# Optimization experiments

Hardware: AMD Instinct MI355X
Metric: run time of the kernel (lower is better)

Reference implementation:

```python
import jax, jax.numpy as jnp
import numpy as np

POSITIVE = 1e-6  # cfg.positive epsilon


def unnormal_gaussian(mask_shape, loc):
    """Unnormalized 2D gaussian per box. loc: [B,N,4] = (cx, cy, w, h) in [0,1].
    Returns [B, N, H, W]."""
    H, W = mask_shape
    cx, cy, w, h = loc[..., 0], loc[..., 1], loc[..., 2], loc[..., 3]
    xs = (jnp.arange(W, dtype=loc.dtype) + 0.5) / W  # [W]
    ys = (jnp.arange(H, dtype=loc.dtype) + 0.5) / H  # [H]
    sx = jnp.maximum(w, 1e-3)[..., None, None]  # [B,N,1,1]
    sy = jnp.maximum(h, 1e-3)[..., None, None]
    dx = xs[None, None, None, :] - cx[..., None, None]  # [B,N,1,W]
    dy = ys[None, None, :, None] - cy[..., None, None]  # [B,N,H,1]
    return jnp.exp(-(dx**2 / (2.0 * sx**2) + dy**2 / (2.0 * sy**2)))


def setup_inputs() -> dict:
    key = jax.random.key(0)
    k1, k2, k3, k4, k5 = jax.random.split(key, 5)
    B, N, K, Hp, Wp, C, H0, W0 = 8, 200, 32, 138, 138, 3, 550, 550
    return {
        "original": jax.random.normal(k1, (B, C, H0, W0), dtype=jnp.float32),
        "loc": jax.random.uniform(k2, (B, N, 4), dtype=jnp.float32),
        "mask": jax.random.normal(k3, (B, N, K), dtype=jnp.float32),
        "conf": jax.random.uniform(k4, (B, N), dtype=jnp.float32),
        "proto": jax.random.normal(k5, (B, Hp, Wp, K), dtype=jnp.float32),
    }


def reference(original, loc, mask, conf, proto):
    original = original.astype(jnp.float32)
    B, C, H0, W0 = original.shape
    Hp, Wp = proto.shape[1], proto.shape[2]
    K = proto.shape[3]

    # gaussian attention window per detection: [B,N,Hp,Wp]
    ug = unnormal_gaussian((Hp, Wp), loc)
    # lincomb of prototypes: [B,N,Hp,Wp]
    assembled = jnp.einsum("bhwk,bnk->bnhw", proto, mask)
    assembled = jax.nn.sigmoid(assembled)
    attention = assembled * ug
    # weight by per-detection confidence: [B,N,Hp,Wp]
    mask_conf = attention * conf[:, :, None, None]
    # normalized squared-confidence reduction over detections: [B,Hp,Wp]
    denom = jnp.sum(mask_conf, axis=1, keepdims=True) + POSITIVE
    final_conf = 1.0 - jnp.sum(mask_conf**2 / denom, axis=1)
    final_conf = jnp.where(jnp.isnan(final_conf), 0.0, final_conf)
    # bilinear resize (align_corners=False == half-pixel centers): [B,H0,W0]
    resized = jax.image.resize(final_conf[:, None], (B, 1, H0, W0), method="linear")[:, 0]
    total_conf = jnp.sum(resized, axis=0)  # [H0,W0]
    weighted_mean = jnp.einsum("bchw,bhw->chw", original, resized) / total_conf
    squared_diff = (original - weighted_mean[None]) ** 2
    weighted_diff = squared_diff * resized[:, None]  # einsum 'abcd,acd->abcd'
    weighted_var = weighted_diff / (total_conf + POSITIVE)
    return jnp.sum(weighted_var) / K * B
```

## Files before the change

### kernel.cpp

```cpp
#include <hip/hip_runtime.h>
#include <math.h>

#define BB   8
#define NDET 200
#define NDP  208
#define NCH  13
#define KK   32
#define HP   138
#define WP   138
#define NXT  9
#define NYP  69
#define NP   (HP*WP)
#define H0   550
#define W0   550
#define NPIX (H0*W0)
#define CC   3
#define POSEPS 1e-6f

typedef __attribute__((ext_vector_type(8))) short  short8;
typedef __attribute__((ext_vector_type(4))) float  floatx4;

#define OFF_AFRAG 0
#define OFF_GX    106496
#define OFF_GYC   1025024
#define OFF_FCONF 1943552

extern "C" __device__ float __builtin_amdgcn_rcpf(float);

__device__ inline unsigned short f32_to_bf16(float f) {
    union { float f; unsigned u; } v; v.f = f;
    unsigned r = v.u + 0x7FFFu + ((v.u >> 16) & 1u);
    return (unsigned short)(r >> 16);
}

__global__ __launch_bounds__(256) void prep_kernel(
    const float* __restrict__ loc,
    const float* __restrict__ conf,
    const float* __restrict__ mask,
    char* __restrict__ ws,
    float* __restrict__ out)
{
    const int idx = blockIdx.x * 256 + threadIdx.x;
    if (idx == 0) out[0] = 0.0f;
    const int W1 = BB * WP * NDP;
    const int W2 = BB * HP * NDP;
    if (idx < W1) {
        int b = idx / (WP * NDP); int r = idx - b * (WP * NDP);
        int x = r / NDP;          int n = r - x * NDP;
        float v = 0.0f;
        if (n < NDET) {
            const float* l = loc + (b * NDET + n) * 4;
            float cx = l[0];
            float w  = fmaxf(l[2], 1e-3f);
            float ia = 1.0f / (2.0f * w * w);
            float dx = (x + 0.5f) * (1.0f / WP) - cx;
            v = __expf(-dx * dx * ia);
        }
        ((float*)(ws + OFF_GX))[idx] = v;
    } else if (idx < W1 + W2) {
        int k = idx - W1;
        int b = k / (HP * NDP); int r = k - b * (HP * NDP);
        int y = r / NDP;        int n = r - y * NDP;
        float v = 0.0f;
        if (n < NDET) {
            const float* l = loc + (b * NDET + n) * 4;
            float cy = l[1];
            float h  = fmaxf(l[3], 1e-3f);
            float ib = 1.0f / (2.0f * h * h);
            float dy = (y + 0.5f) * (1.0f / HP) - cy;
            v = conf[b * NDET + n] * __expf(-dy * dy * ib);
        }
        ((float*)(ws + OFF_GYC))[k] = v;
    } else if (idx < W1 + W2 + BB * NCH * 64) {
        int k = idx - W1 - W2;
        int L = k & 63; int bc = k >> 6;
        int c = bc % NCH; int b = bc / NCH;
        int det = c * 16 + (L & 15);
        int k0  = (L >> 4) * 8;
        unsigned o[4] = {0u, 0u, 0u, 0u};
        if (det < NDET) {
            const float* m = mask + (b * NDET + det) * KK + k0;
#pragma unroll
            for (int j = 0; j < 4; j++) {
                unsigned lo = f32_to_bf16(m[2 * j]);
                unsigned hi = f32_to_bf16(m[2 * j + 1]);
                o[j] = lo | (hi << 16);
            }
        }
        unsigned* dst = (unsigned*)(ws + OFF_AFRAG) + k * 4;
        dst[0] = o[0]; dst[1] = o[1]; dst[2] = o[2]; dst[3] = o[3];
    }
}

__global__ __launch_bounds__(256) void conf_kernel(
    const float* __restrict__ proto,
    const char* __restrict__ ws,
    float* __restrict__ fconf)
{
    const int w   = blockIdx.x * 4 + (threadIdx.x >> 6);
    const int L   = threadIdx.x & 63;
    const int b   = w / (NYP * NXT);
    int rem       = w - b * (NYP * NXT);
    const int yp  = rem / NXT;
    const int xt  = rem - yp * NXT;
    const int y0r = yp * 2, y1r = y0r + 1;
    const int x0  = xt * 16;
    const int q   = L >> 4;
    const int c15 = L & 15;
    const int xl  = min(x0 + c15, WP - 1);

    const short8*  af  = (const short8*)(ws + OFF_AFRAG) + (size_t)b * NCH * 64;
    const floatx4* gx4 = (const floatx4*)(ws + OFF_GX)  + ((size_t)b * WP + xl) * (NDP / 4);
    const floatx4* gy0 = (const floatx4*)(ws + OFF_GYC) + ((size_t)b * HP + y0r) * (NDP / 4);
    const floatx4* gy1 = (const floatx4*)(ws + OFF_GYC) + ((size_t)b * HP + y1r) * (NDP / 4);

    const float* pp0 = proto + (((size_t)b * HP + y0r) * WP + xl) * KK + q * 8;
    const float* pp1 = pp0 + (size_t)WP * KK;
    short8 bf0, bf1;
#pragma unroll
    for (int j = 0; j < 8; j++) {
        bf0[j] = (short)f32_to_bf16(pp0[j]);
        bf1[j] = (short)f32_to_bf16(pp1[j]);
    }

    float s10 = 0.f, s20 = 0.f, s11 = 0.f, s21 = 0.f;
#pragma unroll 2
    for (int c = 0; c < NCH; c++) {
        short8 a = af[c * 64 + L];
        floatx4 d0 = {0.f, 0.f, 0.f, 0.f};
        floatx4 d1 = {0.f, 0.f, 0.f, 0.f};
        d0 = __builtin_amdgcn_mfma_f32_16x16x32_bf16(a, bf0, d0, 0, 0, 0);
        d1 = __builtin_amdgcn_mfma_f32_16x16x32_bf16(a, bf1, d1, 0, 0, 0);
        const floatx4 gxv  = gx4[c * 4 + q];
        const floatx4 gy0v = gy0[c * 4 + q];
        const floatx4 gy1v = gy1[c * 4 + q];
#pragma unroll
        for (int r = 0; r < 4; r++) {
            const float sig0 = __builtin_amdgcn_rcpf(1.0f + __expf(-d0[r]));
            const float mc0  = sig0 * (gxv[r] * gy0v[r]);
            s10 += mc0;
            s20 = fmaf(mc0, mc0, s20);
            const float sig1 = __builtin_amdgcn_rcpf(1.0f + __expf(-d1[r]));
            const float mc1  = sig1 * (gxv[r] * gy1v[r]);
            s11 += mc1;
            s21 = fmaf(mc1, mc1, s21);
        }
    }
    s10 += __shfl_xor(s10, 16, 64); s10 += __shfl_xor(s10, 32, 64);
    s20 += __shfl_xor(s20, 16, 64); s20 += __shfl_xor(s20, 32, 64);
    s11 += __shfl_xor(s11, 16, 64); s11 += __shfl_xor(s11, 32, 64);
    s21 += __shfl_xor(s21, 16, 64); s21 += __shfl_xor(s21, 32, 64);
    if (q == 0 && x0 + c15 < WP) {
        float f0 = 1.0f - s20 / (s10 + POSEPS);
        float f1 = 1.0f - s21 / (s11 + POSEPS);
        if (isnan(f0)) f0 = 0.0f;
        if (isnan(f1)) f1 = 0.0f;
        fconf[((size_t)y0r * WP + x0 + c15) * BB + b] = f0;
        fconf[((size_t)y1r * WP + x0 + c15) * BB + b] = f1;
    }
}

__global__ __launch_bounds__(256) void var_kernel(
    const float* __restrict__ original,
    const float* __restrict__ fconf,
    float* __restrict__ out)
{
    const int i = blockIdx.x;
    const float sc  = (float)HP / (float)H0;
    const float syf = (i + 0.5f) * sc - 0.5f;
    const float fy0 = floorf(syf);
    const float wy  = syf - fy0;
    const int y0 = max((int)fy0, 0);
    const int y1 = min((int)fy0 + 1, HP - 1);

    __shared__ float lds[2 * WP * BB];
    {
        const floatx4* s0 = (const floatx4*)(fconf + (size_t)y0 * WP * BB);
        const floatx4* s1 = (const floatx4*)(fconf + (size_t)y1 * WP * BB);
        floatx4* l4 = (floatx4*)lds;
        for (int t = threadIdx.x; t < WP * 2; t += 256) {
            l4[t] = s0[t];
            l4[WP * 2 + t] = s1[t];
        }
    }
    __syncthreads();
    const floatx4* l4 = (const floatx4*)lds;

    float v = 0.0f;
    for (int j = threadIdx.x; j < W0; j += 256) {
        const float sxf = (j + 0.5f) * sc - 0.5f;
        const float fx0 = floorf(sxf);
        const float wx  = sxf - fx0;
        const int x0 = max((int)fx0, 0);
        const int x1 = min((int)fx0 + 1, WP - 1);

        const floatx4 a00 = l4[x0 * 2],          b00 = l4[x0 * 2 + 1];
        const floatx4 a01 = l4[x1 * 2],          b01 = l4[x1 * 2 + 1];
        const floatx4 a10 = l4[WP * 2 + x0 * 2], b10 = l4[WP * 2 + x0 * 2 + 1];
        const floatx4 a11 = l4[WP * 2 + x1 * 2], b11 = l4[WP * 2 + x1 * 2 + 1];
        const float w00 = (1.0f - wy) * (1.0f - wx);
        const float w01 = (1.0f - wy) * wx;
        const float w10 = wy * (1.0f - wx);
        const float w11 = wy * wx;

        float r[BB];
        float t = 0.0f;
#pragma unroll
        for (int e = 0; e < 4; e++) {
            float rb = w00 * a00[e] + w01 * a01[e] + w10 * a10[e] + w11 * a11[e];
            r[e] = rb; t += rb;
        }
#pragma unroll
        for (int e = 0; e < 4; e++) {
            float rb = w00 * b00[e] + w01 * b01[e] + w10 * b10[e] + w11 * b11[e];
            r[4 + e] = rb; t += rb;
        }
        const float inv_t  = __fdividef(1.0f, t);
        const float inv_te = __fdividef(1.0f, t + POSEPS);
        float acc = 0.0f;
#pragma unroll
        for (int c = 0; c < CC; c++) {
            float sro = 0.0f, sroo = 0.0f;
#pragma unroll
            for (int bb = 0; bb < BB; bb++) {
                const float o  = original[(size_t)(bb * CC + c) * NPIX + (size_t)i * W0 + j];
                const float ro = r[bb] * o;
                sro += ro;
                sroo = fmaf(ro, o, sroo);
            }
            acc += sroo - sro * sro * inv_t;
        }
        v += acc * inv_te;
    }
    for (int off = 32; off > 0; off >>= 1) v += __shfl_down(v, off, 64);
    __shared__ float red[4];
    const int lane = threadIdx.x & 63;
    const int wid  = threadIdx.x >> 6;
    if (lane == 0) red[wid] = v;
    __syncthreads();
    if (threadIdx.x == 0) {
        const float s = red[0] + red[1] + red[2] + red[3];
        atomicAdd(out, s * 0.25f);
    }
}

extern "C" void kernel_launch(void* const* d_in, const int* in_sizes, int n_in,
                              void* d_out, int out_size, void* d_ws, size_t ws_size,
                              hipStream_t stream) {
    const float* original = (const float*)d_in[0];
    const float* loc      = (const float*)d_in[1];
    const float* mask     = (const float*)d_in[2];
    const float* conf     = (const float*)d_in[3];
    const float* proto    = (const float*)d_in[4];
    float* out = (float*)d_out;
    char* ws = (char*)d_ws;
    float* fconf = (float*)(ws + OFF_FCONF);

    const int prep_total = BB * WP * NDP + BB * HP * NDP + BB * NCH * 64;
    prep_kernel<<<(prep_total + 255) / 256, 256, 0, stream>>>(loc, conf, mask, ws, out);

    conf_kernel<<<(BB * NYP * NXT) / 4, 256, 0, stream>>>(proto, ws, fconf);

    var_kernel<<<H0, 256, 0, stream>>>(original, fconf, out);
}
```

Baseline: 114.5 us.

## Store gx table in MFMA-fragment order and split var rows across two blocks

The precomputed x-gaussian table is now written in the same order the MFMA accumulator lanes consume it, so each lane in conf_kernel reads one contiguous floatx4 per chunk with coalesced access instead of strided per-x rows. Workspace offsets shift to fit the larger padded table. var_kernel now launches two blocks per output row, each covering half the columns, which doubles parallelism for the memory-bound variance pass. The cost is redundant LDS staging per half-row and a larger prep write.

```diff
diff --git a/kernel.cpp b/kernel.cpp
--- a/kernel.cpp
+++ b/kernel.cpp
@@ -22,8 +22,8 @@
 
 #define OFF_AFRAG 0
 #define OFF_GX    106496
-#define OFF_GYC   1025024
-#define OFF_FCONF 1943552
+#define OFF_GYC   1064960
+#define OFF_FCONF 1983488
 
 extern "C" __device__ float __builtin_amdgcn_rcpf(float);
 
@@ -42,11 +42,18 @@
 {
     const int idx = blockIdx.x * 256 + threadIdx.x;
     if (idx == 0) out[0] = 0.0f;
-    const int W1 = BB * WP * NDP;
+    const int W1 = BB * NXT * NCH * 64 * 4;
     const int W2 = BB * HP * NDP;
     if (idx < W1) {
-        int b = idx / (WP * NDP); int r = idx - b * (WP * NDP);
-        int x = r / NDP;          int n = r - x * NDP;
+        const int r  = idx & 3;
+        const int L  = (idx >> 2) & 63;
+        const int t  = idx >> 8;
+        const int c  = t % NCH;
+        const int bx = t / NCH;
+        const int xt = bx % NXT;
+        const int b  = bx / NXT;
+        const int n  = c * 16 + (L >> 4) * 4 + r;
+        const int x  = min(xt * 16 + (L & 15), WP - 1);
         float v = 0.0f;
         if (n < NDET) {
             const float* l = loc + (b * NDET + n) * 4;
@@ -109,8 +116,9 @@
     const int c15 = L & 15;
     const int xl  = min(x0 + c15, WP - 1);
 
-    const short8*  af  = (const short8*)(ws + OFF_AFRAG) + (size_t)b * NCH * 64;
-    const floatx4* gx4 = (const floatx4*)(ws + OFF_GX)  + ((size_t)b * WP + xl) * (NDP / 4);
+    const short8*  af  = (const short8*)(ws + OFF_AFRAG) + (size_t)b * NCH * 64 + L;
+    const floatx4* gxf = (const floatx4*)(ws + OFF_GX)
+                         + ((size_t)(b * NXT + xt) * NCH) * 64 + L;
     const floatx4* gy0 = (const floatx4*)(ws + OFF_GYC) + ((size_t)b * HP + y0r) * (NDP / 4);
     const floatx4* gy1 = (const floatx4*)(ws + OFF_GYC) + ((size_t)b * HP + y1r) * (NDP / 4);
 
@@ -126,12 +134,12 @@
     float s10 = 0.f, s20 = 0.f, s11 = 0.f, s21 = 0.f;
 #pragma unroll 2
     for (int c = 0; c < NCH; c++) {
-        short8 a = af[c * 64 + L];
+        short8 a = af[c * 64];
         floatx4 d0 = {0.f, 0.f, 0.f, 0.f};
         floatx4 d1 = {0.f, 0.f, 0.f, 0.f};
         d0 = __builtin_amdgcn_mfma_f32_16x16x32_bf16(a, bf0, d0, 0, 0, 0);
         d1 = __builtin_amdgcn_mfma_f32_16x16x32_bf16(a, bf1, d1, 0, 0, 0);
-        const floatx4 gxv  = gx4[c * 4 + q];
+        const floatx4 gxv  = gxf[c * 64];
         const floatx4 gy0v = gy0[c * 4 + q];
         const floatx4 gy1v = gy1[c * 4 + q];
 #pragma unroll
@@ -165,7 +173,8 @@
     const float* __restrict__ fconf,
     float* __restrict__ out)
 {
-    const int i = blockIdx.x;
+    const int i    = blockIdx.x >> 1;
+    const int half = blockIdx.x & 1;
     const float sc  = (float)HP / (float)H0;
     const float syf = (i + 0.5f) * sc - 0.5f;
     const float fy0 = floorf(syf);
@@ -186,8 +195,10 @@
     __syncthreads();
     const floatx4* l4 = (const floatx4*)lds;
 
+    const int jbeg = half * (W0 / 2);
+    const int jend = jbeg + (W0 / 2);
     float v = 0.0f;
-    for (int j = threadIdx.x; j < W0; j += 256) {
+    for (int j = jbeg + threadIdx.x; j < jend; j += 256) {
         const float sxf = (j + 0.5f) * sc - 0.5f;
         const float fx0 = floorf(sxf);
         const float wx  = sxf - fx0;
@@ -256,10 +267,10 @@
     char* ws = (char*)d_ws;
     float* fconf = (float*)(ws + OFF_FCONF);
 
-    const int prep_total = BB * WP * NDP + BB * HP * NDP + BB * NCH * 64;
+    const int prep_total = BB * NXT * NCH * 64 * 4 + BB * HP * NDP + BB * NCH * 64;
     prep_kernel<<<(prep_total + 255) / 256, 256, 0, stream>>>(loc, conf, mask, ws, out);
 
     conf_kernel<<<(BB * NYP * NXT) / 4, 256, 0, stream>>>(proto, ws, fconf);
 
-    var_kernel<<<H0, 256, 0, stream>>>(original, fconf, out);
-}
+    var_kernel<<<H0 * 2, 256, 0, stream>>>(original, fconf, out);
+}
```

After: 119.7 us. 4.5% more time.
